# Kernel tuning notes

Measured on AMD Instinct MI355X. Metric: run time of the kernel, lower is better.

## Reference

```python
import jax, jax.numpy as jnp
import numpy as np

D_MODEL = 512
NHEAD = 8
D_K = D_MODEL // NHEAD


def setup_inputs() -> dict:
    key = jax.random.key(0)
    ks = jax.random.split(key, 7)
    B, L = 4, 2048
    x = jax.random.normal(ks[0], (B, L, D_MODEL), dtype=jnp.float32)
    scale = 1.0 / np.sqrt(D_MODEL)
    Wq = jax.random.normal(ks[1], (D_MODEL, D_MODEL), dtype=jnp.float32) * scale
    Wk = jax.random.normal(ks[2], (D_MODEL, D_MODEL), dtype=jnp.float32) * scale
    Wv = jax.random.normal(ks[3], (D_MODEL, D_MODEL), dtype=jnp.float32) * scale
    Wo = jax.random.normal(ks[4], (D_MODEL, D_MODEL), dtype=jnp.float32) * scale
    wave_freq = jax.random.normal(ks[5], (NHEAD,), dtype=jnp.float32) * 0.1
    wave_phase = jnp.zeros((NHEAD,), dtype=jnp.float32)
    return {"x": x, "Wq": Wq, "Wk": Wk, "Wv": Wv, "Wo": Wo,
            "wave_freq": wave_freq, "wave_phase": wave_phase}


def reference(x, Wq, Wk, Wv, Wo, wave_freq, wave_phase):
    B, L, D = x.shape
    H, dk = NHEAD, D_K
    # nn.Linear(bias=False): y = x @ W.T
    q = (x @ Wq.T).reshape(B, L, H, dk).transpose(0, 2, 1, 3)  # (B,H,L,dk)
    k = (x @ Wk.T).reshape(B, L, H, dk).transpose(0, 2, 1, 3)
    v = (x @ Wv.T).reshape(B, L, H, dk).transpose(0, 2, 1, 3)
    pos = jnp.arange(L, dtype=x.dtype)  # (L,)
    two_pi = jnp.asarray(2.0 * np.pi, dtype=x.dtype)
    # wave: (H, L) -> broadcast as (1, H, 1, L) over key positions
    wave = jnp.cos(two_pi * wave_freq[:, None] * pos[None, :] + wave_phase[:, None])
    scores = jnp.einsum('bhqd,bhkd->bhqk', q, k) * (dk ** -0.5)
    scores = scores * wave[None, :, None, :]
    attn = jax.nn.softmax(scores, axis=-1)
    out = jnp.einsum('bhqk,bhkd->bhqd', attn, v)
    out = out.transpose(0, 2, 1, 3).reshape(B, L, D)
    return out @ Wo.T
```

## Files before the change

kernel.cpp:

```cpp
#include <hip/hip_runtime.h>
#include <math.h>

#define D_MODEL 512
#define NHEAD   8
#define DK      64
#define BATCH   4
#define SEQ     2048
#define MTOT    (BATCH*SEQ)
#define NXELEM  (MTOT*D_MODEL)
#define NWELEM  (4*D_MODEL*D_MODEL)

typedef _Float16 half8   __attribute__((ext_vector_type(8)));
typedef _Float16 half4_t __attribute__((ext_vector_type(4)));
typedef float    f32x4   __attribute__((ext_vector_type(4)));

#define MFMA32(a,b,c) __builtin_amdgcn_mfma_f32_16x16x32_f16((a),(b),(c),0,0,0)

__global__ __launch_bounds__(256) void cvt_kernel(
    const float* __restrict__ x,
    const float* __restrict__ Wq, const float* __restrict__ Wk,
    const float* __restrict__ Wv, const float* __restrict__ Wo,
    const float* __restrict__ wf, const float* __restrict__ wp,
    _Float16* __restrict__ Xh, _Float16* __restrict__ Wh,
    float* __restrict__ wtab)
{
    const int tid = blockIdx.x * 256 + threadIdx.x;
    int idx = tid * 4;
    if (idx < NXELEM + NWELEM) {
        const float* src; _Float16* dst; int off;
        if (idx < NXELEM) { src = x; dst = Xh; off = idx; }
        else {
            int r = idx - NXELEM;
            int sel = r >> 18;
            off = r & ((1 << 18) - 1);
            src = (sel == 0) ? Wq : (sel == 1) ? Wk : (sel == 2) ? Wv : Wo;
            dst = Wh + ((size_t)sel << 18);
        }
        float4 v = *(const float4*)(src + off);
        half4_t h;
        h[0] = (_Float16)v.x; h[1] = (_Float16)v.y;
        h[2] = (_Float16)v.z; h[3] = (_Float16)v.w;
        *(half4_t*)(dst + off) = h;
    } else {
        int widx = idx - (NXELEM + NWELEM);
        const int h = widx >> 11;
        const int pos0 = widx & 2047;
        const float f  = 6.28318530717958647692f * wf[h];
        const float ph = wp[h];
        float4 o;
        o.x = 0.125f * cosf(fmaf(f, (float)(pos0 + 0), ph));
        o.y = 0.125f * cosf(fmaf(f, (float)(pos0 + 1), ph));
        o.z = 0.125f * cosf(fmaf(f, (float)(pos0 + 2), ph));
        o.w = 0.125f * cosf(fmaf(f, (float)(pos0 + 3), ph));
        *(float4*)(wtab + widx) = o;
    }
}

__global__ __launch_bounds__(256) void qkv_mfma_kernel(
    const _Float16* __restrict__ Xh, const _Float16* __restrict__ Wh,
    const float* __restrict__ wtab,
    _Float16* __restrict__ Qh, _Float16* __restrict__ Kh,
    _Float16* __restrict__ Vth)
{
    __shared__ _Float16 As[128][72];
    __shared__ _Float16 Bs[64][72];

    const int t  = threadIdx.x;
    const int n0 = blockIdx.x * 64;
    const int m0 = blockIdx.y * 128;
    const int which = n0 >> 9;
    const int h = (n0 >> 6) & 7;
    const _Float16* Wbase = Wh + ((size_t)which << 18) + (size_t)(h * 64) * 512;

    const int w = t >> 6, lane = t & 63, ln = lane & 15, quad = lane >> 4;
    const int ar = t >> 1, ac = (t & 1) * 32;
    const int br = t >> 2, bc = (t & 3) * 16;

    const _Float16* ag = Xh + (size_t)(m0 + ar) * 512 + ac;
    const _Float16* bg = Wbase + (size_t)br * 512 + bc;

    const f32x4 kZero = {0.f, 0.f, 0.f, 0.f};
    f32x4 acc[2][4];
    #pragma unroll
    for (int i = 0; i < 2; ++i)
        #pragma unroll
        for (int j = 0; j < 4; ++j) acc[i][j] = kZero;

    for (int k0 = 0; k0 < 512; k0 += 64) {
        half8 av[4], bv[2];
        #pragma unroll
        for (int i = 0; i < 4; ++i) av[i] = *(const half8*)(ag + k0 + i * 8);
        #pragma unroll
        for (int i = 0; i < 2; ++i) bv[i] = *(const half8*)(bg + k0 + i * 8);
        __syncthreads();
        #pragma unroll
        for (int i = 0; i < 4; ++i) *(half8*)&As[ar][ac + i * 8] = av[i];
        #pragma unroll
        for (int i = 0; i < 2; ++i) *(half8*)&Bs[br][bc + i * 8] = bv[i];
        __syncthreads();

        #pragma unroll
        for (int ks = 0; ks < 2; ++ks) {
            half8 af[2], bf[4];
            #pragma unroll
            for (int mt = 0; mt < 2; ++mt)
                af[mt] = *(const half8*)&As[w * 32 + mt * 16 + ln][ks * 32 + quad * 8];
            #pragma unroll
            for (int nt = 0; nt < 4; ++nt)
                bf[nt] = *(const half8*)&Bs[nt * 16 + ln][ks * 32 + quad * 8];
            #pragma unroll
            for (int mt = 0; mt < 2; ++mt)
                #pragma unroll
                for (int nt = 0; nt < 4; ++nt)
                    acc[mt][nt] = MFMA32(af[mt], bf[nt], acc[mt][nt]);
        }
    }

    const int b  = m0 >> 11;
    const int l0 = m0 & 2047;

    if (which < 2) {
        _Float16* dst = (which == 0 ? Qh : Kh) + (size_t)(b * NHEAD + h) * SEQ * DK;
        const float* wt = wtab + h * SEQ;
        #pragma unroll
        for (int mt = 0; mt < 2; ++mt)
            #pragma unroll
            for (int r = 0; r < 4; ++r) {
                const int lq = l0 + w * 32 + mt * 16 + quad * 4 + r;
                const float wv = (which == 1) ? wt[lq] : 1.0f;
                #pragma unroll
                for (int nt = 0; nt < 4; ++nt) {
                    const int d = nt * 16 + ln;
                    dst[(size_t)lq * DK + d] = (_Float16)(acc[mt][nt][r] * wv);
                }
            }
    } else {
        __syncthreads();
        _Float16* Vl = &As[0][0];
        #pragma unroll
        for (int mt = 0; mt < 2; ++mt)
            #pragma unroll
            for (int nt = 0; nt < 4; ++nt)
                #pragma unroll
                for (int r = 0; r < 4; ++r) {
                    const int lq = w * 32 + mt * 16 + quad * 4 + r;
                    const int k32 = lq & 31;
                    const int pos = (lq & ~31) | (((k32 >> 2) & 3) << 3)
                                  | ((k32 >> 4) << 2) | (k32 & 3);
                    const int d  = nt * 16 + ln;
                    Vl[d * 136 + pos] = (_Float16)acc[mt][nt][r];
                }
        __syncthreads();
        _Float16* dst = Vth + (size_t)(b * NHEAD + h) * DK * SEQ;
        const int d = t >> 2, c0 = (t & 3) * 32;
        #pragma unroll
        for (int i = 0; i < 4; ++i) {
            half8 v = *(const half8*)&Vl[d * 136 + c0 + i * 8];
            *(half8*)(dst + (size_t)d * SEQ + l0 + c0 + i * 8) = v;
        }
    }
}

__global__ __launch_bounds__(256) void attn_mfma_kernel(
    const _Float16* __restrict__ Qh, const _Float16* __restrict__ Kwh,
    const _Float16* __restrict__ Vth, _Float16* __restrict__ AOh)
{
    __shared__ _Float16 SM[4][64][72];

    const int bx = blockIdx.x;
    const int g8 = bx & 7;
    const int s  = bx >> 3;
    const int bh = g8 * 4 + (s >> 4);
    const int q0 = (s & 15) * 128;
    const int b = bh >> 3, h = bh & 7;

    const int t = threadIdx.x;
    const int w = t >> 6, lane = t & 63, ln = lane & 15, quad = lane >> 4;

    const _Float16* Qg = Qh + ((size_t)bh * SEQ + q0) * DK;
    const _Float16* Kg = Kwh + (size_t)bh * SEQ * DK;
    const _Float16* Vg = Vth + (size_t)bh * DK * SEQ;

    const int sr = t >> 2, sc = (t & 3) * 16;
    const int qr = t >> 1, qc = (t & 1) * 32;

    {
        const _Float16* qp = Qg + (size_t)qr * DK + qc;
        half8 qv0 = *(const half8*)(qp);
        half8 qv1 = *(const half8*)(qp + 8);
        half8 qv2 = *(const half8*)(qp + 16);
        half8 qv3 = *(const half8*)(qp + 24);
        const _Float16* kp = Kg + (size_t)sr * DK + sc;
        const _Float16* vp = Vg + (size_t)sr * SEQ + sc;
        half8 kv0 = *(const half8*)(kp);
        half8 kv1 = *(const half8*)(kp + 8);
        half8 vv0 = *(const half8*)(vp);
        half8 vv1 = *(const half8*)(vp + 8);
        _Float16* qd = &SM[2 + (qr >> 6)][qr & 63][qc];
        *(half8*)(qd)      = qv0;
        *(half8*)(qd + 8)  = qv1;
        *(half8*)(qd + 16) = qv2;
        *(half8*)(qd + 24) = qv3;
        *(half8*)&SM[0][sr][sc]     = kv0;
        *(half8*)&SM[0][sr][sc + 8] = kv1;
        *(half8*)&SM[1][sr][sc]     = vv0;
        *(half8*)&SM[1][sr][sc + 8] = vv1;
    }
    __syncthreads();

    half8 qf[2][2];
    #pragma unroll
    for (int u = 0; u < 2; ++u) {
        const int row = w * 32 + u * 16 + ln;
        const _Float16* qsrc = &SM[2 + (row >> 6)][row & 63][0];
        qf[u][0] = *(const half8*)(qsrc + quad * 8);
        qf[u][1] = *(const half8*)(qsrc + 32 + quad * 8);
    }
    __syncthreads();

    const f32x4 kZero = {0.f, 0.f, 0.f, 0.f};
    f32x4 o[2][4];
    #pragma unroll
    for (int u = 0; u < 2; ++u)
        #pragma unroll
        for (int nt = 0; nt < 4; ++nt) o[u][nt] = kZero;
    float l_acc[2] = {0.f, 0.f};

    for (int kt = 0; kt < SEQ / 64; ++kt) {
        const int cur = kt & 1;

        half8 pk0, pk1, pv0, pv1;
        const bool more = (kt + 1 < SEQ / 64);
        if (more) {
            const _Float16* kp = Kg + (size_t)((kt + 1) * 64 + sr) * DK + sc;
            const _Float16* vp = Vg + (size_t)sr * SEQ + (kt + 1) * 64 + sc;
            pk0 = *(const half8*)(kp);
            pk1 = *(const half8*)(kp + 8);
            pv0 = *(const half8*)(vp);
            pv1 = *(const half8*)(vp + 8);
        }

        const _Float16 (*Ks)[72] = SM[2 * cur];
        const _Float16 (*Vs)[72] = SM[2 * cur + 1];

        #pragma unroll
        for (int g = 0; g < 2; ++g) {
            half8 ka0 = *(const half8*)&Ks[(2 * g + 0) * 16 + ln][quad * 8];
            half8 ka1 = *(const half8*)&Ks[(2 * g + 0) * 16 + ln][32 + quad * 8];
            half8 kb0 = *(const half8*)&Ks[(2 * g + 1) * 16 + ln][quad * 8];
            half8 kb1 = *(const half8*)&Ks[(2 * g + 1) * 16 + ln][32 + quad * 8];
            half8 vf[4];
            #pragma unroll
            for (int nt = 0; nt < 4; ++nt)
                vf[nt] = *(const half8*)&Vs[nt * 16 + ln][g * 32 + quad * 8];

            #pragma unroll
            for (int u = 0; u < 2; ++u) {
                f32x4 s0 = MFMA32(ka0, qf[u][0], kZero);
                f32x4 s1 = MFMA32(kb0, qf[u][0], kZero);
                s0 = MFMA32(ka1, qf[u][1], s0);
                s1 = MFMA32(kb1, qf[u][1], s1);

                half8 pf;
                float ps = 0.f;
                #pragma unroll
                for (int r = 0; r < 4; ++r) {
                    const float e0 = __expf(s0[r]);
                    const float e1 = __expf(s1[r]);
                    pf[r]     = (_Float16)e0;
                    pf[r + 4] = (_Float16)e1;
                    ps += e0 + e1;
                }
                l_acc[u] += ps;

                #pragma unroll
                for (int nt = 0; nt < 4; ++nt)
                    o[u][nt] = MFMA32(pf, vf[nt], o[u][nt]);
            }
        }

        __syncthreads();
        if (more) {
            _Float16* kd = &SM[2 * (cur ^ 1)][sr][sc];
            _Float16* vd = &SM[2 * (cur ^ 1) + 1][sr][sc];
            *(half8*)(kd)     = pk0;
            *(half8*)(kd + 8) = pk1;
            *(half8*)(vd)     = pv0;
            *(half8*)(vd + 8) = pv1;
        }
        __syncthreads();
    }

    #pragma unroll
    for (int u = 0; u < 2; ++u) {
        l_acc[u] += __shfl_xor(l_acc[u], 16);
        l_acc[u] += __shfl_xor(l_acc[u], 32);
    }

    #pragma unroll
    for (int u = 0; u < 2; ++u)
        #pragma unroll
        for (int r = 0; r < 4; ++r) {
            const float lr  = __shfl(l_acc[u], quad * 4 + r, 16);
            const float inv = 1.0f / lr;
            const int lq = q0 + w * 32 + u * 16 + quad * 4 + r;
            const size_t base = ((size_t)b * SEQ + lq) * D_MODEL + h * DK;
            #pragma unroll
            for (int nt = 0; nt < 4; ++nt)
                AOh[base + nt * 16 + ln] = (_Float16)(o[u][nt][r] * inv);
        }
}

__global__ __launch_bounds__(256) void out_mfma_kernel(
    const _Float16* __restrict__ AOh, const _Float16* __restrict__ Woh,
    float* __restrict__ out)
{
    __shared__ _Float16 As[128][72];
    __shared__ _Float16 Bs[64][72];

    const int t  = threadIdx.x;
    const int n0 = blockIdx.x * 64;
    const int m0 = blockIdx.y * 128;

    const int w = t >> 6, lane = t & 63, ln = lane & 15, quad = lane >> 4;
    const int ar = t >> 1, ac = (t & 1) * 32;
    const int br = t >> 2, bc = (t & 3) * 16;

    const _Float16* ag = AOh + (size_t)(m0 + ar) * 512 + ac;
    const _Float16* bg = Woh + (size_t)(n0 + br) * 512 + bc;

    const f32x4 kZero = {0.f, 0.f, 0.f, 0.f};
    f32x4 acc[2][4];
    #pragma unroll
    for (int i = 0; i < 2; ++i)
        #pragma unroll
        for (int j = 0; j < 4; ++j) acc[i][j] = kZero;

    for (int k0 = 0; k0 < 512; k0 += 64) {
        half8 av[4], bv[2];
        #pragma unroll
        for (int i = 0; i < 4; ++i) av[i] = *(const half8*)(ag + k0 + i * 8);
        #pragma unroll
        for (int i = 0; i < 2; ++i) bv[i] = *(const half8*)(bg + k0 + i * 8);
        __syncthreads();
        #pragma unroll
        for (int i = 0; i < 4; ++i) *(half8*)&As[ar][ac + i * 8] = av[i];
        #pragma unroll
        for (int i = 0; i < 2; ++i) *(half8*)&Bs[br][bc + i * 8] = bv[i];
        __syncthreads();

        #pragma unroll
        for (int ks = 0; ks < 2; ++ks) {
            half8 af[2], bf[4];
            #pragma unroll
            for (int mt = 0; mt < 2; ++mt)
                af[mt] = *(const half8*)&As[w * 32 + mt * 16 + ln][ks * 32 + quad * 8];
            #pragma unroll
            for (int nt = 0; nt < 4; ++nt)
                bf[nt] = *(const half8*)&Bs[nt * 16 + ln][ks * 32 + quad * 8];
            #pragma unroll
            for (int mt = 0; mt < 2; ++mt)
                #pragma unroll
                for (int nt = 0; nt < 4; ++nt)
                    acc[mt][nt] = MFMA32(af[mt], bf[nt], acc[mt][nt]);
        }
    }

    #pragma unroll
    for (int mt = 0; mt < 2; ++mt)
        #pragma unroll
        for (int nt = 0; nt < 4; ++nt)
            #pragma unroll
            for (int r = 0; r < 4; ++r) {
                const int gm = m0 + w * 32 + mt * 16 + quad * 4 + r;
                out[(size_t)gm * 512 + n0 + nt * 16 + ln] = acc[mt][nt][r];
            }
}

extern "C" void kernel_launch(void* const* d_in, const int* in_sizes, int n_in,
                              void* d_out, int out_size, void* d_ws, size_t ws_size,
                              hipStream_t stream)
{
    (void)in_sizes; (void)n_in; (void)out_size; (void)ws_size;
    const float* x  = (const float*)d_in[0];
    const float* Wq = (const float*)d_in[1];
    const float* Wk = (const float*)d_in[2];
    const float* Wv = (const float*)d_in[3];
    const float* Wo = (const float*)d_in[4];
    const float* wf = (const float*)d_in[5];
    const float* wp = (const float*)d_in[6];
    float* out = (float*)d_out;

    const size_t NX = (size_t)MTOT * D_MODEL;
    _Float16* Xh  = (_Float16*)d_ws;
    _Float16* Wh  = Xh + NX;
    _Float16* Qh  = Wh + 4 * 262144;
    _Float16* Kh  = Qh + NX;
    _Float16* Vth = Kh + NX;
    _Float16* AOh = Vth + NX;
    float*    wtab = (float*)(AOh + NX);

    cvt_kernel<<<5136, 256, 0, stream>>>(x, Wq, Wk, Wv, Wo, wf, wp, Xh, Wh, wtab);

    dim3 g1(24, 64);
    qkv_mfma_kernel<<<g1, 256, 0, stream>>>(Xh, Wh, wtab, Qh, Kh, Vth);

    attn_mfma_kernel<<<512, 256, 0, stream>>>(Qh, Kh, Vth, AOh);

    dim3 g3(8, 64);
    out_mfma_kernel<<<g3, 256, 0, stream>>>(AOh, Wh + 3 * 262144, out);
}
```

Before: 168.4 us.

## Stage GEMM epilogues through LDS for coalesced stores and use exp2 softmax

The Q/K projection epilogue and the output projection epilogue now write their accumulators to shared memory first, then issue wide, coalesced vector stores to global memory. Before, each lane made scattered scalar stores. The V transpose epilogue now packs eight halves per LDS write instead of doing per-element permuted writes. In attention, the log2(e) factor is folded into the precomputed wave table, so exp2 can be used directly, and probabilities are converted with packed round-toward-zero conversions. The price is extra barriers and LDS traffic. The float4 LDS reads at a 66-float row stride may also be misaligned on odd rows.

Result: no change. 167.2 us (-0.7%).

```diff
diff --git a/kernel.cpp b/kernel.cpp
--- a/kernel.cpp
+++ b/kernel.cpp
@@ -12,9 +12,12 @@
 
 typedef _Float16 half8   __attribute__((ext_vector_type(8)));
 typedef _Float16 half4_t __attribute__((ext_vector_type(4)));
+typedef __fp16   fp16x2  __attribute__((ext_vector_type(2)));
 typedef float    f32x4   __attribute__((ext_vector_type(4)));
 
 #define MFMA32(a,b,c) __builtin_amdgcn_mfma_f32_16x16x32_f16((a),(b),(c),0,0,0)
+
+#define WSCALE 0.18033688011117130f
 
 __global__ __launch_bounds__(256) void cvt_kernel(
     const float* __restrict__ x,
@@ -48,10 +51,10 @@
         const float f  = 6.28318530717958647692f * wf[h];
         const float ph = wp[h];
         float4 o;
-        o.x = 0.125f * cosf(fmaf(f, (float)(pos0 + 0), ph));
-        o.y = 0.125f * cosf(fmaf(f, (float)(pos0 + 1), ph));
-        o.z = 0.125f * cosf(fmaf(f, (float)(pos0 + 2), ph));
-        o.w = 0.125f * cosf(fmaf(f, (float)(pos0 + 3), ph));
+        o.x = WSCALE * cosf(fmaf(f, (float)(pos0 + 0), ph));
+        o.y = WSCALE * cosf(fmaf(f, (float)(pos0 + 1), ph));
+        o.z = WSCALE * cosf(fmaf(f, (float)(pos0 + 2), ph));
+        o.w = WSCALE * cosf(fmaf(f, (float)(pos0 + 3), ph));
         *(float4*)(wtab + widx) = o;
     }
 }
@@ -122,41 +125,46 @@
     if (which < 2) {
         _Float16* dst = (which == 0 ? Qh : Kh) + (size_t)(b * NHEAD + h) * SEQ * DK;
         const float* wt = wtab + h * SEQ;
+        __syncthreads();
+        _Float16* Ql = &As[0][0];
         #pragma unroll
         for (int mt = 0; mt < 2; ++mt)
             #pragma unroll
             for (int r = 0; r < 4; ++r) {
-                const int lq = l0 + w * 32 + mt * 16 + quad * 4 + r;
-                const float wv = (which == 1) ? wt[lq] : 1.0f;
-                #pragma unroll
-                for (int nt = 0; nt < 4; ++nt) {
-                    const int d = nt * 16 + ln;
-                    dst[(size_t)lq * DK + d] = (_Float16)(acc[mt][nt][r] * wv);
-                }
+                const int lr = w * 32 + mt * 16 + quad * 4 + r;
+                const float wv = (which == 1) ? wt[l0 + lr] : 1.0f;
+                #pragma unroll
+                for (int nt = 0; nt < 4; ++nt)
+                    Ql[lr * 72 + nt * 16 + ln] = (_Float16)(acc[mt][nt][r] * wv);
             }
+        __syncthreads();
+        #pragma unroll
+        for (int rr = 0; rr < 4; ++rr) {
+            const int row = rr * 32 + (t >> 3);
+            half8 v = *(const half8*)&Ql[row * 72 + (t & 7) * 8];
+            *(half8*)(dst + (size_t)(l0 + row) * DK + (t & 7) * 8) = v;
+        }
     } else {
         __syncthreads();
         _Float16* Vl = &As[0][0];
         #pragma unroll
-        for (int mt = 0; mt < 2; ++mt)
-            #pragma unroll
-            for (int nt = 0; nt < 4; ++nt)
-                #pragma unroll
-                for (int r = 0; r < 4; ++r) {
-                    const int lq = w * 32 + mt * 16 + quad * 4 + r;
-                    const int k32 = lq & 31;
-                    const int pos = (lq & ~31) | (((k32 >> 2) & 3) << 3)
-                                  | ((k32 >> 4) << 2) | (k32 & 3);
-                    const int d  = nt * 16 + ln;
-                    Vl[d * 136 + pos] = (_Float16)acc[mt][nt][r];
-                }
+        for (int nt = 0; nt < 4; ++nt) {
+            half8 hv;
+            #pragma unroll
+            for (int mt = 0; mt < 2; ++mt)
+                #pragma unroll
+                for (int r = 0; r < 4; ++r)
+                    hv[mt * 4 + r] = (_Float16)acc[mt][nt][r];
+            const int d = nt * 16 + ln;
+            *(half8*)&Vl[d * 136 + w * 32 + quad * 8] = hv;
+        }
         __syncthreads();
         _Float16* dst = Vth + (size_t)(b * NHEAD + h) * DK * SEQ;
-        const int d = t >> 2, c0 = (t & 3) * 32;
-        #pragma unroll
-        for (int i = 0; i < 4; ++i) {
-            half8 v = *(const half8*)&Vl[d * 136 + c0 + i * 8];
-            *(half8*)(dst + (size_t)d * SEQ + l0 + c0 + i * 8) = v;
+        #pragma unroll
+        for (int rr = 0; rr < 4; ++rr) {
+            const int d = rr * 16 + (t >> 4);
+            half8 v = *(const half8*)&Vl[d * 136 + (t & 15) * 8];
+            *(half8*)(dst + (size_t)d * SEQ + l0 + (t & 15) * 8) = v;
         }
     }
 }
@@ -261,21 +269,24 @@
                 s0 = MFMA32(ka1, qf[u][1], s0);
                 s1 = MFMA32(kb1, qf[u][1], s1);
 
-                half8 pf;
-                float ps = 0.f;
-                #pragma unroll
-                for (int r = 0; r < 4; ++r) {
-                    const float e0 = __expf(s0[r]);
-                    const float e1 = __expf(s1[r]);
-                    pf[r]     = (_Float16)e0;
-                    pf[r + 4] = (_Float16)e1;
-                    ps += e0 + e1;
-                }
-                l_acc[u] += ps;
+                const float e00 = __builtin_amdgcn_exp2f(s0[0]);
+                const float e01 = __builtin_amdgcn_exp2f(s0[1]);
+                const float e02 = __builtin_amdgcn_exp2f(s0[2]);
+                const float e03 = __builtin_amdgcn_exp2f(s0[3]);
+                const float e10 = __builtin_amdgcn_exp2f(s1[0]);
+                const float e11 = __builtin_amdgcn_exp2f(s1[1]);
+                const float e12 = __builtin_amdgcn_exp2f(s1[2]);
+                const float e13 = __builtin_amdgcn_exp2f(s1[3]);
+                union { half8 v; fp16x2 h2[4]; } pu;
+                pu.h2[0] = __builtin_amdgcn_cvt_pkrtz(e00, e01);
+                pu.h2[1] = __builtin_amdgcn_cvt_pkrtz(e02, e03);
+                pu.h2[2] = __builtin_amdgcn_cvt_pkrtz(e10, e11);
+                pu.h2[3] = __builtin_amdgcn_cvt_pkrtz(e12, e13);
+                l_acc[u] += ((e00 + e01) + (e02 + e03)) + ((e10 + e11) + (e12 + e13));
 
                 #pragma unroll
                 for (int nt = 0; nt < 4; ++nt)
-                    o[u][nt] = MFMA32(pf, vf[nt], o[u][nt]);
+                    o[u][nt] = MFMA32(pu.v, vf[nt], o[u][nt]);
             }
         }
 
@@ -366,15 +377,30 @@
         }
     }
 
-    #pragma unroll
-    for (int mt = 0; mt < 2; ++mt)
-        #pragma unroll
-        for (int nt = 0; nt < 4; ++nt)
-            #pragma unroll
-            for (int r = 0; r < 4; ++r) {
-                const int gm = m0 + w * 32 + mt * 16 + quad * 4 + r;
-                out[(size_t)gm * 512 + n0 + nt * 16 + ln] = acc[mt][nt][r];
-            }
+    float* Os = (float*)&As[0][0];
+    #pragma unroll
+    for (int pass = 0; pass < 2; ++pass) {
+        __syncthreads();
+        if ((w >> 1) == pass) {
+            const int rbase = (w & 1) * 32;
+            #pragma unroll
+            for (int mt = 0; mt < 2; ++mt)
+                #pragma unroll
+                for (int r = 0; r < 4; ++r) {
+                    const int row = rbase + mt * 16 + quad * 4 + r;
+                    #pragma unroll
+                    for (int nt = 0; nt < 4; ++nt)
+                        Os[row * 66 + nt * 16 + ln] = acc[mt][nt][r];
+                }
+        }
+        __syncthreads();
+        #pragma unroll
+        for (int rr = 0; rr < 4; ++rr) {
+            const int row = rr * 16 + (t >> 4);
+            float4 v = *(const float4*)&Os[row * 66 + (t & 15) * 4];
+            *(float4*)(out + (size_t)(m0 + pass * 64 + row) * 512 + n0 + (t & 15) * 4) = v;
+        }
+    }
 }
 
 extern "C" void kernel_launch(void* const* d_in, const int* in_sizes, int n_in,
```
